# Kernel tuning notes

Hardware: AMD Instinct MI355X
Metric: run time of the kernel (lower is better)

Reference implementation:

```python
import jax, jax.numpy as jnp
import numpy as np

FFT_LEN = 512
HOP = 256
WIN_LEN = 1024


def setup_inputs() -> dict:
    key = jax.random.key(0)
    k1, k2 = jax.random.split(key)
    inputs = jax.random.normal(k1, (8, 514, 4000), dtype=jnp.float32)
    win = jax.random.uniform(k2, (WIN_LEN,), dtype=jnp.float32)
    return {"inputs": inputs, "win": win}


def reference(inputs, win):
    B, D, T = inputs.shape  # D == 514
    half = FFT_LEN // 2  # 256
    real = inputs[:, :half, :]            # [B,256,T]
    imag = inputs[:, half + 1:-1, :]      # [B,256,T]
    c = jax.lax.complex(real, imag)       # bins 0..255
    # conjugate-symmetric extension: bin 256 = 0, bins 257..511 = conj(bins 255..1)
    tail = jnp.conj(jnp.flip(c[:, 1:, :], axis=1))            # [B,255,T]
    zero = jnp.zeros_like(c[:, :1, :])
    spec = jnp.concatenate([c, zero, tail], axis=1)           # [B,512,T]
    # torch does fft over the freq axis and keeps the real part
    ifft_data = jnp.real(jnp.fft.fft(spec, axis=1)).astype(jnp.float32)  # [B,512,T]
    tmp = jnp.concatenate([ifft_data, ifft_data], axis=1)     # [B,1024,T]
    tmp = tmp * win[None, :, None] * 256.0
    # overlap-add via four shifted padded copies (faithful to the original)
    t1 = jnp.pad(tmp, ((0, 0), (0, 768), (0, 3)))
    t2 = jnp.pad(tmp, ((0, 0), (256, 512), (1, 2)))
    t3 = jnp.pad(tmp, ((0, 0), (512, 256), (2, 1)))
    t4 = jnp.pad(tmp, ((0, 0), (768, 0), (3, 0)))
    synbuf = t1 + t2 + t3 + t4                                # [B,1792,T+3]
    syn = synbuf[:, 768:1024, :-4]                            # [B,256,T-1]
    syn = jnp.flip(syn, axis=1)
    syn = jnp.transpose(syn, (0, 2, 1)).reshape(B, -1)        # [B,256*(T-1)]
    return syn
```

## Files before the change

### kernel.cpp

```cpp
#include <hip/hip_runtime.h>


typedef __attribute__((ext_vector_type(8))) short short8;
typedef __attribute__((ext_vector_type(8))) __bf16 bf16x8;
typedef __attribute__((ext_vector_type(4))) float floatx4;

__device__ inline short f2bf(float f) {
  unsigned u = __builtin_bit_cast(unsigned, f);
  u = (u + 0x7fffu + ((u >> 16) & 1u)) >> 16;
  return (short)(unsigned short)u;
}

#define PI_OVER_256 0.01227184630308513f

__global__ void build_m(short* __restrict__ M) {
  int idx = blockIdx.x * blockDim.x + threadIdx.x;
  int ntile = idx >> 10;
  int s = (idx >> 6) & 15;
  int lane = idx & 63;
  int n = ntile * 16 + (lane & 15);
  int kb = lane >> 4;
  short8 v;
#pragma unroll
  for (int e = 0; e < 8; e++) {
    int kap = s * 32 + kb * 8 + e;
    int gk = 2 * (kap & 255) + (kap >> 8);
    float val;
    if (gk == 0) {
      val = 1.0f;
    } else if (gk < 256) {
      int m = (n * gk) & 511;
      val = 2.0f * __cosf((float)m * PI_OVER_256);
    } else {
      int m = (n * (gk - 256)) & 511;
      val = 2.0f * __sinf((float)m * PI_OVER_256);
    }
    v[e] = f2bf(val);
  }
  ((short8*)M)[idx] = v;
}

__global__ __launch_bounds__(512, 4) void gemm_ola(
    const float* __restrict__ in, const float* __restrict__ win,
    const short* __restrict__ M, float* __restrict__ out) {
  __shared__ short ldsX[64 * 512];

  const int tid = threadIdx.x;
  const int b = blockIdx.y;
  const int tile = blockIdx.x;
  const int c0 = 60 * tile - 4;

  {
    const int cbase = 4 * (tid & 15);
    const int gc = c0 + cbase;
    const bool ok = (gc >= 0 && gc <= 3996);
    const float* src = in + (size_t)b * 2056000 + gc;
#pragma unroll
    for (int pass = 0; pass < 2; pass++) {
      const int kap0 = (tid >> 4) * 8 + pass * 256;
      floatx4 f[8];
      if (ok) {
#pragma unroll
        for (int j = 0; j < 8; j++) {
          int kap = kap0 + j;
          int gk = 2 * (kap & 255) + (kap >> 8);
          int row = (gk < 256) ? gk : gk + 1;
          f[j] = *(const floatx4*)(src + (size_t)row * 4000);
        }
      } else {
#pragma unroll
        for (int j = 0; j < 8; j++) f[j] = floatx4{0.f, 0.f, 0.f, 0.f};
      }
      const int g = kap0 >> 3;
#pragma unroll
      for (int cc = 0; cc < 4; cc++) {
        short8 v;
#pragma unroll
        for (int j = 0; j < 8; j++) v[j] = f2bf(f[j][cc]);
        const int col = cbase + cc;
        *(short8*)&ldsX[col * 512 + ((g ^ (col & 7)) << 3)] = v;
      }
    }
  }
  __syncthreads();

  const int w = tid >> 6;
  const int lane = tid & 63;
  const int c = lane & 15;
  const int kb = lane >> 4;
  const int rg = kb;

  floatx4 accE[4][2] = {};
  floatx4 accO[4][2] = {};

  const short8* Mf = (const short8*)M;
  const int J0 = 2 * w, J1 = 2 * w + 1;

  bf16x8 cb0 = __builtin_bit_cast(bf16x8, Mf[(J0 * 16 + 0) * 64 + lane]);
  bf16x8 cb1 = __builtin_bit_cast(bf16x8, Mf[(J1 * 16 + 0) * 64 + lane]);

#pragma unroll
  for (int s = 0; s < 16; s++) {
    bf16x8 nb0, nb1;
    if (s < 15) {
      nb0 = __builtin_bit_cast(bf16x8, Mf[(J0 * 16 + s + 1) * 64 + lane]);
      nb1 = __builtin_bit_cast(bf16x8, Mf[(J1 * 16 + s + 1) * 64 + lane]);
    }
    const int g = 4 * s + kb;
    bf16x8 a[4];
#pragma unroll
    for (int q = 0; q < 4; q++) {
      const int col = 16 * q + c;
      a[q] = __builtin_bit_cast(
          bf16x8, *(const short8*)&ldsX[col * 512 + ((g ^ (col & 7)) << 3)]);
    }
    if (s < 8) {
#pragma unroll
      for (int q = 0; q < 4; q++) {
        accE[q][0] = __builtin_amdgcn_mfma_f32_16x16x32_bf16(a[q], cb0, accE[q][0], 0, 0, 0);
        accE[q][1] = __builtin_amdgcn_mfma_f32_16x16x32_bf16(a[q], cb1, accE[q][1], 0, 0, 0);
      }
    } else {
#pragma unroll
      for (int q = 0; q < 4; q++) {
        accO[q][0] = __builtin_amdgcn_mfma_f32_16x16x32_bf16(a[q], cb0, accO[q][0], 0, 0, 0);
        accO[q][1] = __builtin_amdgcn_mfma_f32_16x16x32_bf16(a[q], cb1, accO[q][1], 0, 0, 0);
      }
    }
    if (s < 15) { cb0 = nb0; cb1 = nb1; }
  }

#pragma unroll
  for (int jt = 0; jt < 2; jt++) {
    const int J = 2 * w + jt;
    const int j = 16 * J + c;
    const float wv0 = 256.0f * win[768 + j];
    const float wv1 = 256.0f * win[512 + j];
    const float wv2 = 256.0f * win[256 + j];
    const float wv3 = 256.0f * win[j];

    floatx4 Y[4], Yh[4];
#pragma unroll
    for (int q = 0; q < 4; q++) {
      Y[q] = accE[q][jt] + accO[q][jt];
      Yh[q] = accE[q][jt] - accO[q][jt];
    }

#pragma unroll
    for (int q = 0; q < 4; q++) {
      const int qm = (q > 0) ? q - 1 : 0;
      float yb[4], yhb[4];
#pragma unroll
      for (int p = 1; p < 4; p++) {
        float ia = __shfl(Y[q][p], lane - 16, 64);
        float pa = __shfl(Y[qm][p], lane + 48, 64);
        yb[p] = (rg > 0) ? ia : pa;
      }
#pragma unroll
      for (int p = 2; p < 4; p++) {
        float ia = __shfl(Yh[q][p], lane - 16, 64);
        float pa = __shfl(Yh[qm][p], lane + 48, 64);
        yhb[p] = (rg > 0) ? ia : pa;
      }
      floatx4 v;
#pragma unroll
      for (int p = 0; p < 4; p++) {
        float t1 = (p >= 1) ? Y[q][p - 1] : yb[3];
        float t2 = (p >= 2) ? Yh[q][p - 2] : yhb[p + 2];
        float t3 = (p >= 3) ? Y[q][p - 3] : yb[p + 1];
        v[p] = wv0 * Yh[q][p] + wv1 * t1 + wv2 * t2 + wv3 * t3;
      }
#pragma unroll
      for (int p = 0; p < 4; p++) {
        const int L = 16 * q + 4 * rg + p;
        const int t = c0 + L;
        if (L >= 4 && t <= 3998) {
          out[((size_t)b * 3999 + t) * 256 + (255 - j)] = v[p];
        }
      }
    }
  }
}

extern "C" void kernel_launch(void* const* d_in, const int* in_sizes, int n_in,
                              void* d_out, int out_size, void* d_ws, size_t ws_size,
                              hipStream_t stream) {
  const float* in = (const float*)d_in[0];
  const float* win = (const float*)d_in[1];
  float* out = (float*)d_out;
  short* M = (short*)d_ws;

  hipLaunchKernelGGL(build_m, dim3(64), dim3(256), 0, stream, M);
  hipLaunchKernelGGL(gemm_ola, dim3(67, 8), dim3(512), 0, stream, in, win, M, out);
}
```

Baseline: 116.8 us.

## Make GEMM-OLA kernel persistent with register-prefetched next tile

Launches one block per CU (256 blocks), and each block loops over time tiles with stride 32. The next tile's input rows are loaded into registers while the current tile's MFMAs and overlap-add run, then written to LDS between barriers. This hides global-load latency without relying on multiple resident blocks. It costs a large register prefetch buffer and a lower launch-bounds occupancy target, and tile counts per block are uneven (2 or 3).

```diff
diff --git a/kernel.cpp b/kernel.cpp
--- a/kernel.cpp
+++ b/kernel.cpp
@@ -40,144 +40,173 @@
   ((short8*)M)[idx] = v;
 }
 
-__global__ __launch_bounds__(512, 4) void gemm_ola(
+__global__ __launch_bounds__(512, 2) void gemm_ola(
     const float* __restrict__ in, const float* __restrict__ win,
     const short* __restrict__ M, float* __restrict__ out) {
   __shared__ short ldsX[64 * 512];
 
   const int tid = threadIdx.x;
-  const int b = blockIdx.y;
-  const int tile = blockIdx.x;
-  const int c0 = 60 * tile - 4;
-
-  {
-    const int cbase = 4 * (tid & 15);
-    const int gc = c0 + cbase;
-    const bool ok = (gc >= 0 && gc <= 3996);
-    const float* src = in + (size_t)b * 2056000 + gc;
-#pragma unroll
-    for (int pass = 0; pass < 2; pass++) {
-      const int kap0 = (tid >> 4) * 8 + pass * 256;
-      floatx4 f[8];
-      if (ok) {
-#pragma unroll
-        for (int j = 0; j < 8; j++) {
-          int kap = kap0 + j;
-          int gk = 2 * (kap & 255) + (kap >> 8);
-          int row = (gk < 256) ? gk : gk + 1;
-          f[j] = *(const floatx4*)(src + (size_t)row * 4000);
-        }
-      } else {
-#pragma unroll
-        for (int j = 0; j < 8; j++) f[j] = floatx4{0.f, 0.f, 0.f, 0.f};
-      }
-      const int g = kap0 >> 3;
-#pragma unroll
-      for (int cc = 0; cc < 4; cc++) {
-        short8 v;
-#pragma unroll
-        for (int j = 0; j < 8; j++) v[j] = f2bf(f[j][cc]);
-        const int col = cbase + cc;
-        *(short8*)&ldsX[col * 512 + ((g ^ (col & 7)) << 3)] = v;
-      }
-    }
-  }
-  __syncthreads();
+  const int bid = blockIdx.x;
+  const int b = bid & 7;
+  const int t0 = bid >> 3;
+
+  const int cbase = 4 * (tid & 15);
+  const int kg = tid >> 4;
+  const float* srcb = in + (size_t)b * 2056000;
 
   const int w = tid >> 6;
   const int lane = tid & 63;
   const int c = lane & 15;
-  const int kb = lane >> 4;
-  const int rg = kb;
-
-  floatx4 accE[4][2] = {};
-  floatx4 accO[4][2] = {};
-
+  const int rg = lane >> 4;
   const short8* Mf = (const short8*)M;
   const int J0 = 2 * w, J1 = 2 * w + 1;
 
-  bf16x8 cb0 = __builtin_bit_cast(bf16x8, Mf[(J0 * 16 + 0) * 64 + lane]);
-  bf16x8 cb1 = __builtin_bit_cast(bf16x8, Mf[(J1 * 16 + 0) * 64 + lane]);
-
-#pragma unroll
-  for (int s = 0; s < 16; s++) {
-    bf16x8 nb0, nb1;
-    if (s < 15) {
-      nb0 = __builtin_bit_cast(bf16x8, Mf[(J0 * 16 + s + 1) * 64 + lane]);
-      nb1 = __builtin_bit_cast(bf16x8, Mf[(J1 * 16 + s + 1) * 64 + lane]);
-    }
-    const int g = 4 * s + kb;
-    bf16x8 a[4];
-#pragma unroll
-    for (int q = 0; q < 4; q++) {
-      const int col = 16 * q + c;
-      a[q] = __builtin_bit_cast(
-          bf16x8, *(const short8*)&ldsX[col * 512 + ((g ^ (col & 7)) << 3)]);
-    }
-    if (s < 8) {
+  float wv[2][4];
+#pragma unroll
+  for (int jt = 0; jt < 2; jt++) {
+    const int j = 16 * (2 * w + jt) + c;
+    wv[jt][0] = 256.0f * win[768 + j];
+    wv[jt][1] = 256.0f * win[512 + j];
+    wv[jt][2] = 256.0f * win[256 + j];
+    wv[jt][3] = 256.0f * win[j];
+  }
+
+  floatx4 f[2][8];
+
+  auto load_f = [&](int tile_) {
+    const int gc = 60 * tile_ - 4 + cbase;
+    if (gc >= 0 && gc <= 3996) {
+      const float* src = srcb + gc;
+#pragma unroll
+      for (int p = 0; p < 2; p++)
+#pragma unroll
+        for (int j = 0; j < 8; j++) {
+          const int kk = kg * 8 + j;
+          const int gk = 2 * kk + p;
+          const int row = (gk < 256) ? gk : gk + 1;
+          f[p][j] = *(const floatx4*)(src + (size_t)row * 4000);
+        }
+    } else {
+#pragma unroll
+      for (int p = 0; p < 2; p++)
+#pragma unroll
+        for (int j = 0; j < 8; j++) f[p][j] = floatx4{0.f, 0.f, 0.f, 0.f};
+    }
+  };
+
+  auto write_lds = [&]() {
+#pragma unroll
+    for (int p = 0; p < 2; p++) {
+      const int g = kg + 32 * p;
+#pragma unroll
+      for (int cc = 0; cc < 4; cc++) {
+        short8 v;
+#pragma unroll
+        for (int j = 0; j < 8; j++) v[j] = f2bf(f[p][j][cc]);
+        const int col = cbase + cc;
+        *(short8*)&ldsX[col * 512 + ((g ^ (col & 7)) << 3)] = v;
+      }
+    }
+  };
+
+  load_f(t0);
+  write_lds();
+  __syncthreads();
+
+  for (int tile = t0; tile < 67; tile += 32) {
+    const int c0 = 60 * tile - 4;
+    const bool have_next = (tile + 32) < 67;
+
+    if (have_next) load_f(tile + 32);
+
+    floatx4 accE[4][2] = {};
+    floatx4 accO[4][2] = {};
+
+    bf16x8 cb0 = __builtin_bit_cast(bf16x8, Mf[(J0 * 16 + 0) * 64 + lane]);
+    bf16x8 cb1 = __builtin_bit_cast(bf16x8, Mf[(J1 * 16 + 0) * 64 + lane]);
+
+#pragma unroll
+    for (int s = 0; s < 16; s++) {
+      bf16x8 nb0, nb1;
+      if (s < 15) {
+        nb0 = __builtin_bit_cast(bf16x8, Mf[(J0 * 16 + s + 1) * 64 + lane]);
+        nb1 = __builtin_bit_cast(bf16x8, Mf[(J1 * 16 + s + 1) * 64 + lane]);
+      }
+      const int g = 4 * s + rg;
+      bf16x8 a[4];
 #pragma unroll
       for (int q = 0; q < 4; q++) {
-        accE[q][0] = __builtin_amdgcn_mfma_f32_16x16x32_bf16(a[q], cb0, accE[q][0], 0, 0, 0);
-        accE[q][1] = __builtin_amdgcn_mfma_f32_16x16x32_bf16(a[q], cb1, accE[q][1], 0, 0, 0);
-      }
-    } else {
+        const int col = 16 * q + c;
+        a[q] = __builtin_bit_cast(
+            bf16x8, *(const short8*)&ldsX[col * 512 + ((g ^ (c & 7)) << 3)]);
+      }
+      if (s < 8) {
+#pragma unroll
+        for (int q = 0; q < 4; q++) {
+          accE[q][0] = __builtin_amdgcn_mfma_f32_16x16x32_bf16(a[q], cb0, accE[q][0], 0, 0, 0);
+          accE[q][1] = __builtin_amdgcn_mfma_f32_16x16x32_bf16(a[q], cb1, accE[q][1], 0, 0, 0);
+        }
+      } else {
+#pragma unroll
+        for (int q = 0; q < 4; q++) {
+          accO[q][0] = __builtin_amdgcn_mfma_f32_16x16x32_bf16(a[q], cb0, accO[q][0], 0, 0, 0);
+          accO[q][1] = __builtin_amdgcn_mfma_f32_16x16x32_bf16(a[q], cb1, accO[q][1], 0, 0, 0);
+        }
+      }
+      if (s < 15) { cb0 = nb0; cb1 = nb1; }
+    }
+
+#pragma unroll
+    for (int jt = 0; jt < 2; jt++) {
+      const int j = 16 * (2 * w + jt) + c;
+
+      floatx4 Y[4], Yh[4];
 #pragma unroll
       for (int q = 0; q < 4; q++) {
-        accO[q][0] = __builtin_amdgcn_mfma_f32_16x16x32_bf16(a[q], cb0, accO[q][0], 0, 0, 0);
-        accO[q][1] = __builtin_amdgcn_mfma_f32_16x16x32_bf16(a[q], cb1, accO[q][1], 0, 0, 0);
-      }
-    }
-    if (s < 15) { cb0 = nb0; cb1 = nb1; }
-  }
-
-#pragma unroll
-  for (int jt = 0; jt < 2; jt++) {
-    const int J = 2 * w + jt;
-    const int j = 16 * J + c;
-    const float wv0 = 256.0f * win[768 + j];
-    const float wv1 = 256.0f * win[512 + j];
-    const float wv2 = 256.0f * win[256 + j];
-    const float wv3 = 256.0f * win[j];
-
-    floatx4 Y[4], Yh[4];
-#pragma unroll
-    for (int q = 0; q < 4; q++) {
-      Y[q] = accE[q][jt] + accO[q][jt];
-      Yh[q] = accE[q][jt] - accO[q][jt];
-    }
-
-#pragma unroll
-    for (int q = 0; q < 4; q++) {
-      const int qm = (q > 0) ? q - 1 : 0;
-      float yb[4], yhb[4];
-#pragma unroll
-      for (int p = 1; p < 4; p++) {
-        float ia = __shfl(Y[q][p], lane - 16, 64);
-        float pa = __shfl(Y[qm][p], lane + 48, 64);
-        yb[p] = (rg > 0) ? ia : pa;
-      }
-#pragma unroll
-      for (int p = 2; p < 4; p++) {
-        float ia = __shfl(Yh[q][p], lane - 16, 64);
-        float pa = __shfl(Yh[qm][p], lane + 48, 64);
-        yhb[p] = (rg > 0) ? ia : pa;
-      }
-      floatx4 v;
-#pragma unroll
-      for (int p = 0; p < 4; p++) {
-        float t1 = (p >= 1) ? Y[q][p - 1] : yb[3];
-        float t2 = (p >= 2) ? Yh[q][p - 2] : yhb[p + 2];
-        float t3 = (p >= 3) ? Y[q][p - 3] : yb[p + 1];
-        v[p] = wv0 * Yh[q][p] + wv1 * t1 + wv2 * t2 + wv3 * t3;
-      }
-#pragma unroll
-      for (int p = 0; p < 4; p++) {
-        const int L = 16 * q + 4 * rg + p;
-        const int t = c0 + L;
-        if (L >= 4 && t <= 3998) {
-          out[((size_t)b * 3999 + t) * 256 + (255 - j)] = v[p];
-        }
-      }
+        Y[q] = accE[q][jt] + accO[q][jt];
+        Yh[q] = accE[q][jt] - accO[q][jt];
+      }
+
+#pragma unroll
+      for (int q = 0; q < 4; q++) {
+        const int qm = (q > 0) ? q - 1 : 0;
+        float yb[4], yhb[4];
+#pragma unroll
+        for (int p = 1; p < 4; p++) {
+          float ia = __shfl(Y[q][p], lane - 16, 64);
+          float pa = __shfl(Y[qm][p], lane + 48, 64);
+          yb[p] = (rg > 0) ? ia : pa;
+        }
+#pragma unroll
+        for (int p = 2; p < 4; p++) {
+          float ia = __shfl(Yh[q][p], lane - 16, 64);
+          float pa = __shfl(Yh[qm][p], lane + 48, 64);
+          yhb[p] = (rg > 0) ? ia : pa;
+        }
+        floatx4 v;
+#pragma unroll
+        for (int p = 0; p < 4; p++) {
+          float t1 = (p >= 1) ? Y[q][p - 1] : yb[3];
+          float t2 = (p >= 2) ? Yh[q][p - 2] : yhb[p + 2];
+          float t3 = (p >= 3) ? Y[q][p - 3] : yb[p + 1];
+          v[p] = wv[jt][0] * Yh[q][p] + wv[jt][1] * t1 + wv[jt][2] * t2 +
+                 wv[jt][3] * t3;
+        }
+#pragma unroll
+        for (int p = 0; p < 4; p++) {
+          const int L = 16 * q + 4 * rg + p;
+          const int t = c0 + L;
+          if (L >= 4 && t <= 3998) {
+            out[((size_t)b * 3999 + t) * 256 + (255 - j)] = v[p];
+          }
+        }
+      }
+    }
+
+    if (have_next) {
+      __syncthreads();
+      write_lds();
+      __syncthreads();
     }
   }
 }
@@ -191,5 +220,5 @@
   short* M = (short*)d_ws;
 
   hipLaunchKernelGGL(build_m, dim3(64), dim3(256), 0, stream, M);
-  hipLaunchKernelGGL(gemm_ola, dim3(67, 8), dim3(512), 0, stream, in, win, M, out);
-}
+  hipLaunchKernelGGL(gemm_ola, dim3(256), dim3(512), 0, stream, in, win, M, out);
+}
```

Result: slower. 154.2 us (+32.0%).

## Warp-specialize GEMM with producer waves double-buffering input chunks in LDS

Applied to the files above, without the earlier changes.

Doubles the block to 1024 threads: the upper 512 threads act as producers that load and bf16-convert 128-row K chunks into a double-buffered LDS region, while the lower 512 threads run the MFMA loop on the previous chunk. This is meant to overlap global loads with matrix compute instead of staging the whole 512-deep tile before any math starts. It shrinks LDS per block, which may allow more resident blocks. The cost is one extra barrier per chunk, narrower 8-byte loads, and idle producer waves during the epilogue.

```diff
diff --git a/kernel.cpp b/kernel.cpp
--- a/kernel.cpp
+++ b/kernel.cpp
@@ -4,6 +4,7 @@
 typedef __attribute__((ext_vector_type(8))) short short8;
 typedef __attribute__((ext_vector_type(8))) __bf16 bf16x8;
 typedef __attribute__((ext_vector_type(4))) float floatx4;
+typedef __attribute__((ext_vector_type(2))) float floatx2;
 
 __device__ inline short f2bf(float f) {
   unsigned u = __builtin_bit_cast(unsigned, f);
@@ -40,100 +41,112 @@
   ((short8*)M)[idx] = v;
 }
 
-__global__ __launch_bounds__(512, 4) void gemm_ola(
+__global__ __launch_bounds__(1024, 4) void gemm_ola(
     const float* __restrict__ in, const float* __restrict__ win,
     const short* __restrict__ M, float* __restrict__ out) {
-  __shared__ short ldsX[64 * 512];
+  __shared__ short ldsB[2][64 * 128];
 
   const int tid = threadIdx.x;
   const int b = blockIdx.y;
   const int tile = blockIdx.x;
   const int c0 = 60 * tile - 4;
 
-  {
-    const int cbase = 4 * (tid & 15);
-    const int gc = c0 + cbase;
-    const bool ok = (gc >= 0 && gc <= 3996);
-    const float* src = in + (size_t)b * 2056000 + gc;
-#pragma unroll
-    for (int pass = 0; pass < 2; pass++) {
-      const int kap0 = (tid >> 4) * 8 + pass * 256;
-      floatx4 f[8];
-      if (ok) {
-#pragma unroll
-        for (int j = 0; j < 8; j++) {
-          int kap = kap0 + j;
-          int gk = 2 * (kap & 255) + (kap >> 8);
-          int row = (gk < 256) ? gk : gk + 1;
-          f[j] = *(const floatx4*)(src + (size_t)row * 4000);
-        }
-      } else {
-#pragma unroll
-        for (int j = 0; j < 8; j++) f[j] = floatx4{0.f, 0.f, 0.f, 0.f};
-      }
-      const int g = kap0 >> 3;
-#pragma unroll
-      for (int cc = 0; cc < 4; cc++) {
-        short8 v;
-#pragma unroll
-        for (int j = 0; j < 8; j++) v[j] = f2bf(f[j][cc]);
-        const int col = cbase + cc;
-        *(short8*)&ldsX[col * 512 + ((g ^ (col & 7)) << 3)] = v;
-      }
-    }
-  }
-  __syncthreads();
+  const bool producer = (tid >= 512);
+
+  const int pp = tid & 511;
+  const int cp = pp & 31;
+  const int pkg = pp >> 5;
+  const int pgc = c0 + 2 * cp;
+  const bool pok = (pgc >= 0 && pgc <= 3998);
+  const float* psrc = in + (size_t)b * 2056000 + pgc;
 
   const int w = tid >> 6;
   const int lane = tid & 63;
   const int c = lane & 15;
-  const int kb = lane >> 4;
-  const int rg = kb;
+  const int rg = lane >> 4;
+  const short8* Mf = (const short8*)M;
+  const int J0 = 2 * w, J1 = 2 * w + 1;
+
+#define STAGE(CH)                                                           \
+  {                                                                         \
+    floatx2 f[8];                                                           \
+    if (pok) {                                                              \
+      _Pragma("unroll") for (int e = 0; e < 8; e++) {                       \
+        const int kap = (CH) * 128 + pkg * 8 + e;                           \
+        const int gk = 2 * (kap & 255) + (kap >> 8);                        \
+        const int row = (gk < 256) ? gk : gk + 1;                           \
+        f[e] = *(const floatx2*)(psrc + (size_t)row * 4000);                \
+      }                                                                     \
+    } else {                                                                \
+      _Pragma("unroll") for (int e = 0; e < 8; e++) f[e] = floatx2{0.f, 0.f}; \
+    }                                                                       \
+    _Pragma("unroll") for (int cc = 0; cc < 2; cc++) {                      \
+      short8 v;                                                             \
+      _Pragma("unroll") for (int e = 0; e < 8; e++) v[e] = f2bf(f[e][cc]);  \
+      const int col = 2 * cp + cc;                                          \
+      *(short8*)&ldsB[(CH) & 1][col * 128 + ((pkg ^ (col & 7)) << 3)] = v;  \
+    }                                                                       \
+  }
 
   floatx4 accE[4][2] = {};
   floatx4 accO[4][2] = {};
-
-  const short8* Mf = (const short8*)M;
-  const int J0 = 2 * w, J1 = 2 * w + 1;
-
-  bf16x8 cb0 = __builtin_bit_cast(bf16x8, Mf[(J0 * 16 + 0) * 64 + lane]);
-  bf16x8 cb1 = __builtin_bit_cast(bf16x8, Mf[(J1 * 16 + 0) * 64 + lane]);
-
-#pragma unroll
-  for (int s = 0; s < 16; s++) {
-    bf16x8 nb0, nb1;
-    if (s < 15) {
-      nb0 = __builtin_bit_cast(bf16x8, Mf[(J0 * 16 + s + 1) * 64 + lane]);
-      nb1 = __builtin_bit_cast(bf16x8, Mf[(J1 * 16 + s + 1) * 64 + lane]);
-    }
-    const int g = 4 * s + kb;
-    bf16x8 a[4];
-#pragma unroll
-    for (int q = 0; q < 4; q++) {
-      const int col = 16 * q + c;
-      a[q] = __builtin_bit_cast(
-          bf16x8, *(const short8*)&ldsX[col * 512 + ((g ^ (col & 7)) << 3)]);
-    }
-    if (s < 8) {
-#pragma unroll
-      for (int q = 0; q < 4; q++) {
-        accE[q][0] = __builtin_amdgcn_mfma_f32_16x16x32_bf16(a[q], cb0, accE[q][0], 0, 0, 0);
-        accE[q][1] = __builtin_amdgcn_mfma_f32_16x16x32_bf16(a[q], cb1, accE[q][1], 0, 0, 0);
-      }
+  bf16x8 cb0, cb1;
+
+  if (producer) {
+    STAGE(0);
+  } else {
+    cb0 = __builtin_bit_cast(bf16x8, Mf[(J0 * 16 + 0) * 64 + lane]);
+    cb1 = __builtin_bit_cast(bf16x8, Mf[(J1 * 16 + 0) * 64 + lane]);
+  }
+  __syncthreads();
+
+#pragma unroll
+  for (int ch = 0; ch < 4; ch++) {
+    if (producer) {
+      if (ch < 3) STAGE(ch + 1);
     } else {
 #pragma unroll
-      for (int q = 0; q < 4; q++) {
-        accO[q][0] = __builtin_amdgcn_mfma_f32_16x16x32_bf16(a[q], cb0, accO[q][0], 0, 0, 0);
-        accO[q][1] = __builtin_amdgcn_mfma_f32_16x16x32_bf16(a[q], cb1, accO[q][1], 0, 0, 0);
-      }
-    }
-    if (s < 15) { cb0 = nb0; cb1 = nb1; }
-  }
+      for (int si = 0; si < 4; si++) {
+        const int s = 4 * ch + si;
+        bf16x8 nb0, nb1;
+        if (s < 15) {
+          nb0 = __builtin_bit_cast(bf16x8, Mf[(J0 * 16 + s + 1) * 64 + lane]);
+          nb1 = __builtin_bit_cast(bf16x8, Mf[(J1 * 16 + s + 1) * 64 + lane]);
+        }
+        const int gl = 4 * si + rg;
+        bf16x8 a[4];
+#pragma unroll
+        for (int q = 0; q < 4; q++) {
+          const int col = 16 * q + c;
+          a[q] = __builtin_bit_cast(
+              bf16x8,
+              *(const short8*)&ldsB[ch & 1][col * 128 + ((gl ^ (c & 7)) << 3)]);
+        }
+        if (s < 8) {
+#pragma unroll
+          for (int q = 0; q < 4; q++) {
+            accE[q][0] = __builtin_amdgcn_mfma_f32_16x16x32_bf16(a[q], cb0, accE[q][0], 0, 0, 0);
+            accE[q][1] = __builtin_amdgcn_mfma_f32_16x16x32_bf16(a[q], cb1, accE[q][1], 0, 0, 0);
+          }
+        } else {
+#pragma unroll
+          for (int q = 0; q < 4; q++) {
+            accO[q][0] = __builtin_amdgcn_mfma_f32_16x16x32_bf16(a[q], cb0, accO[q][0], 0, 0, 0);
+            accO[q][1] = __builtin_amdgcn_mfma_f32_16x16x32_bf16(a[q], cb1, accO[q][1], 0, 0, 0);
+          }
+        }
+        if (s < 15) { cb0 = nb0; cb1 = nb1; }
+      }
+    }
+    __syncthreads();
+  }
+#undef STAGE
+
+  if (producer) return;
 
 #pragma unroll
   for (int jt = 0; jt < 2; jt++) {
-    const int J = 2 * w + jt;
-    const int j = 16 * J + c;
+    const int j = 16 * (2 * w + jt) + c;
     const float wv0 = 256.0f * win[768 + j];
     const float wv1 = 256.0f * win[512 + j];
     const float wv2 = 256.0f * win[256 + j];
@@ -191,5 +204,5 @@
   short* M = (short*)d_ws;
 
   hipLaunchKernelGGL(build_m, dim3(64), dim3(256), 0, stream, M);
-  hipLaunchKernelGGL(gemm_ola, dim3(67, 8), dim3(512), 0, stream, in, win, M, out);
-}
+  hipLaunchKernelGGL(gemm_ola, dim3(67, 8), dim3(1024), 0, stream, in, win, M, out);
+}
```

Measured after the change: 120.5 us. 3.2% more time.
